# Performance work log

Hardware: AMD Instinct MI355X
Metric: run time of the kernel (lower is better)

## Reference

```python
import jax, jax.numpy as jnp
import numpy as np
import math

N = 50_000       # points (CSR segments)
V = 500_000      # mapped views (ragged rows)
IN_MAIN, IN_MAP, IN_MOD = 64, 16, 128
NC, NC_QK = 32, 8
EPS = 1e-12


def setup_inputs() -> dict:
    key = jax.random.key(0)
    ks = jax.random.split(key, 18)
    def rn(k, shape, fan_in=None):
        s = (1.0 / math.sqrt(fan_in)) if fan_in else 1.0
        return jax.random.normal(k, shape, jnp.float32) * s
    x_main = rn(ks[0], (N, IN_MAIN))
    x_mod = rn(ks[1], (V, IN_MOD))
    x_map = rn(ks[2], (V, IN_MAP))
    # CSR pointers: monotone, csr[0]=0, csr[-1]=V (full row coverage)
    inner = jnp.sort(jax.random.randint(ks[3], (N - 1,), 0, V))
    csr_idx = jnp.concatenate([jnp.zeros(1, jnp.int32), inner.astype(jnp.int32),
                               jnp.full((1,), V, jnp.int32)])
    return {
        "x_main": x_main, "x_mod": x_mod, "x_map": x_map, "csr_idx": csr_idx,
        # E_main: MLP([in_main, nc, nc], bias=False)
        "W_main1": rn(ks[4], (IN_MAIN, NC), IN_MAIN),
        "W_main2": rn(ks[5], (NC, NC), NC),
        # E_map (DeepSetFeat): elementwise MLP + segment-max set context + fuse
        "W_map1": rn(ks[6], (IN_MAP, NC), IN_MAP),
        "W_map2": rn(ks[7], (2 * NC, NC), 2 * NC),
        # E_mod: MLP([in_mod, in_mod, in_mod], bias=False)
        "W_mod1": rn(ks[8], (IN_MOD, IN_MOD), IN_MOD),
        "W_mod2": rn(ks[9], (IN_MOD, IN_MOD), IN_MOD),
        # Q, K linear heads (nc_inner -> nc_qk * num_groups), with bias
        "WQ": rn(ks[10], (NC, NC_QK), NC), "bQ": jnp.zeros((NC_QK,), jnp.float32),
        "WK": rn(ks[11], (NC, NC_QK), NC), "bK": jnp.zeros((NC_QK,), jnp.float32),
        # Gating(num_groups=1): weight init ones, bias init zeros
        "g_w": jnp.ones((1, 1), jnp.float32), "g_b": jnp.zeros((1, 1), jnp.float32),
    }


def reference(x_main, x_mod, x_map, csr_idx,
              W_main1, W_main2, W_map1, W_map2, W_mod1, W_mod2,
              WQ, bQ, WK, bK, g_w, g_b):
    counts = csr_idx[1:] - csr_idx[:-1]                     # [N]
    dense_idx = jnp.repeat(jnp.arange(N, dtype=jnp.int32), counts,
                           total_repeat_length=V)           # [V]
    nonempty = counts > 0                                   # [N]

    # --- encoders ---
    h_main = jax.nn.relu(x_main @ W_main1) @ W_main2        # [N, NC]
    h = jax.nn.relu(x_map @ W_map1)                         # [V, NC]
    set_ctx = jax.ops.segment_max(h, dense_idx, num_segments=N)
    set_ctx = jnp.where(nonempty[:, None], set_ctx, 0.0)    # empty segs -> 0
    h_map = jax.nn.relu(jnp.concatenate([h, set_ctx[dense_idx]], axis=1) @ W_map2)  # [V, NC]
    h_mod = jax.nn.relu(x_mod @ W_mod1) @ W_mod2            # [V, IN_MOD]

    # --- Q/K compatibilities (num_groups=1) ---
    keys = h_map @ WK + bK                                  # [V, NC_QK]
    queries = (h_main @ WQ + bQ)[dense_idx]                 # [V, NC_QK]
    comp = jnp.sum(keys * queries, axis=1) / jnp.sqrt(jnp.float32(NC_QK))  # [V]

    # --- segment_softmax_csr ---
    seg_max = jax.ops.segment_max(comp, dense_idx, num_segments=N)
    seg_max = jnp.where(nonempty, seg_max, 0.0)
    cexp = jnp.exp(comp - seg_max[dense_idx])               # [V]
    seg_sum = jax.ops.segment_sum(cexp, dense_idx, num_segments=N) + EPS
    att = cexp / seg_sum[dense_idx]                         # [V]

    # --- attention-weighted pooling ---
    x_pool = jax.ops.segment_sum(h_mod * att[:, None], dense_idx, num_segments=N)  # [N, IN_MOD]

    # --- gating on per-segment max compatibility ---
    gate_in = jnp.where(nonempty, seg_max, 0.0)[:, None]    # [N, 1]
    gate = jnp.tanh(jax.nn.relu(g_w * gate_in + g_b))       # [N, 1]
    x_pool = x_pool * gate

    x_seen = nonempty
    return x_pool, x_seen
```

## Files before the change

### kernel.cpp

```cpp
#include <hip/hip_runtime.h>
#include <math.h>

#define N_PTS 50000
#define V_VIEWS 500000
#define IN_MAIN 64
#define IN_MAP 16
#define IN_MOD 128
#define NC 32
#define NC_QK 8
#define SEG_EPS 1e-12f

typedef short bf16x8 __attribute__((ext_vector_type(8)));
typedef float f32x4 __attribute__((ext_vector_type(4)));

static __device__ __forceinline__ short f2bf(float x) {
    union { float f; unsigned u; } v; v.f = x;
    unsigned r = v.u + 0x7fffu + ((v.u >> 16) & 1u);
    return (short)(r >> 16);
}


__global__ __launch_bounds__(256) void k0_setup(const int* __restrict__ csr,
                                                const float* __restrict__ Wmod1,
                                                const float* __restrict__ Wmod2,
                                                const float* __restrict__ Wm1,
                                                const float* __restrict__ Wm2,
                                                int* __restrict__ didx,
                                                float* __restrict__ pooled,
                                                float* __restrict__ ctxw,
                                                short* __restrict__ Wf,
                                                short* __restrict__ W1f,
                                                short* __restrict__ W2af,
                                                short* __restrict__ W2f) {
    int t = blockIdx.x * blockDim.x + threadIdx.x;
    int total = gridDim.x * blockDim.x;
    if (t < N_PTS) {
        int a = csr[t], b = csr[t + 1];
        for (int v = a; v < b; ++v) didx[v] = t;
    }
    for (int i = t; i < N_PTS * IN_MOD; i += total) pooled[i] = 0.f;
    for (int i = t; i < N_PTS * NC; i += total) ctxw[i] = 0.f;
    for (int i = t; i < IN_MOD * IN_MOD; i += total) {
        int e = i & 7, l = (i >> 3) & 63, j = (i >> 9) & 7, kk = i >> 12;
        int k = kk * 32 + ((l >> 4) << 3) + e;
        int ch = (j << 4) + (l & 15);
        Wf[i] = f2bf(Wmod1[k * IN_MOD + ch]);
        W2f[i] = f2bf(Wmod2[k * IN_MOD + ch]);
    }
    for (int i = t; i < 1024; i += total) {
        int e = i & 7, l = (i >> 3) & 63, j = i >> 9;
        int k = ((l >> 4) << 3) + e;
        int ch = (j << 4) + (l & 15);
        W1f[i] = (k < IN_MAP) ? f2bf(Wm1[k * NC + ch]) : (short)0;
        W2af[i] = f2bf(Wm2[k * NC + ch]);
    }
}

__global__ __launch_bounds__(256) void kA_main_q(
    const float* __restrict__ x_main, const float* __restrict__ W1,
    const float* __restrict__ W2, const float* __restrict__ WQ,
    const float* __restrict__ bQ, const float* __restrict__ WK,
    const float* __restrict__ bK,
    float* __restrict__ wq, float* __restrict__ qb) {
    __shared__ float W1l[IN_MAIN * NC];
    __shared__ float W2l[NC * NC];
    __shared__ float WQl[NC * NC_QK];
    __shared__ float WKl[NC * NC_QK];
    __shared__ float bQl[NC_QK];
    __shared__ float bKl[NC_QK];
    __shared__ float h1buf[8][NC];
    __shared__ float h2buf[8][NC];
    __shared__ float qbuf[8][NC_QK];
    int tid = threadIdx.x;
    for (int i = tid; i < IN_MAIN * NC; i += 256) W1l[i] = W1[i];
    for (int i = tid; i < NC * NC; i += 256) W2l[i] = W2[i];
    for (int i = tid; i < NC * NC_QK; i += 256) WQl[i] = WQ[i];
    for (int i = tid; i < NC * NC_QK; i += 256) WKl[i] = WK[i];
    if (tid < NC_QK) { bQl[tid] = bQ[tid]; bKl[tid] = bK[tid]; }
    __syncthreads();
    int g = tid >> 5, c = tid & 31;
    int p = blockIdx.x * 8 + g;
    float h1 = 0.f;
    if (p < N_PTS) {
        const float* xr = x_main + (size_t)p * IN_MAIN;
        for (int k = 0; k < IN_MAIN; ++k) h1 += xr[k] * W1l[k * NC + c];
        h1 = fmaxf(h1, 0.f);
    }
    h1buf[g][c] = h1;
    __syncthreads();
    float h2 = 0.f;
    for (int j = 0; j < NC; ++j) h2 += h1buf[g][j] * W2l[j * NC + c];
    h2buf[g][c] = h2;
    __syncthreads();
    if (c < NC_QK) {
        float acc = bQl[c];
        for (int j = 0; j < NC; ++j) acc += h2buf[g][j] * WQl[j * NC_QK + c];
        qbuf[g][c] = acc;
    }
    __syncthreads();
    if (p < N_PTS) {
        float w = 0.f;
        for (int j = 0; j < NC_QK; ++j) w += WKl[c * NC_QK + j] * qbuf[g][j];
        wq[(size_t)p * NC + c] = w;
        if (c == 0) {
            float b = 0.f;
            for (int j = 0; j < NC_QK; ++j) b += bKl[j] * qbuf[g][j];
            qb[p] = b;
        }
    }
}

__global__ __launch_bounds__(256) void kH_ctx(
    const float* __restrict__ x_map, const int* __restrict__ didx,
    const short* __restrict__ W1f, int* __restrict__ ctxbits,
    short* __restrict__ hbuf) {
    __shared__ float hl[4][16 * 36];
    int tid = threadIdx.x;
    int w = tid >> 6, lane = tid & 63;
    int vbase = blockIdx.x * 64 + w * 16;
    if (vbase >= V_VIEWS) return;
    const bf16x8* pW1 = (const bf16x8*)W1f;
    bf16x8 b1a = pW1[lane], b1b = pW1[64 + lane];

    bf16x8 a1 = (bf16x8){0, 0, 0, 0, 0, 0, 0, 0};
    if (lane < 32) {
        const float* xp = x_map + (size_t)(vbase + (lane & 15)) * IN_MAP + ((lane >> 4) << 3);
        float4 x0 = *(const float4*)xp;
        float4 x1 = *(const float4*)(xp + 4);
        a1[0] = f2bf(x0.x); a1[1] = f2bf(x0.y); a1[2] = f2bf(x0.z); a1[3] = f2bf(x0.w);
        a1[4] = f2bf(x1.x); a1[5] = f2bf(x1.y); a1[6] = f2bf(x1.z); a1[7] = f2bf(x1.w);
    }
    f32x4 d1a = (f32x4){0.f, 0.f, 0.f, 0.f}, d1b = (f32x4){0.f, 0.f, 0.f, 0.f};
    d1a = __builtin_amdgcn_mfma_f32_16x16x32_bf16(a1, b1a, d1a, 0, 0, 0);
    d1b = __builtin_amdgcn_mfma_f32_16x16x32_bf16(a1, b1b, d1b, 0, 0, 0);

    int c = lane & 15, kq = lane >> 4;
    int vr0 = kq << 2;
    float* hw = hl[w];
#pragma unroll
    for (int r = 0; r < 4; ++r) {
        hw[(vr0 + r) * 36 + c] = fmaxf(d1a[r], 0.f);
        hw[(vr0 + r) * 36 + c + 16] = fmaxf(d1b[r], 0.f);
    }
    const float* hr = hw + c * 36 + (kq << 3);
    float4 h0 = *(const float4*)hr;
    float4 h1 = *(const float4*)(hr + 4);
    bf16x8 a2;
    a2[0] = f2bf(h0.x); a2[1] = f2bf(h0.y); a2[2] = f2bf(h0.z); a2[3] = f2bf(h0.w);
    a2[4] = f2bf(h1.x); a2[5] = f2bf(h1.y); a2[6] = f2bf(h1.z); a2[7] = f2bf(h1.w);
    *(bf16x8*)(hbuf + (size_t)(vbase + c) * NC + (kq << 3)) = a2;

    int vg = vbase + vr0;
    int4 ss = *(const int4*)(didx + vg);
    const int* sp = (const int*)&ss;
    float ma = 0.f, mb = 0.f;
#pragma unroll
    for (int r = 0; r < 4; ++r) {
        ma = fmaxf(ma, fmaxf(d1a[r], 0.f));
        mb = fmaxf(mb, fmaxf(d1b[r], 0.f));
        bool runend = (r == 3) || (sp[r + 1] != sp[r]);
        if (runend) {
            atomicMax(&ctxbits[sp[r] * NC + c], __float_as_int(ma));
            atomicMax(&ctxbits[sp[r] * NC + c + 16], __float_as_int(mb));
            ma = 0.f; mb = 0.f;
        }
    }
}

__global__ __launch_bounds__(256) void kB2b_ctxw(
    const float* __restrict__ Wm2, float* __restrict__ ctxw) {
    __shared__ float W2bl[NC * NC];
    __shared__ float ctxl[8][NC];
    int tid = threadIdx.x;
    for (int i = tid; i < NC * NC; i += 256) W2bl[i] = Wm2[NC * NC + i];
    int g = tid >> 5, c = tid & 31;
    int s = blockIdx.x * 8 + g;
    float cv = (s < N_PTS) ? ctxw[(size_t)s * NC + c] : 0.f;
    ctxl[g][c] = cv;
    __syncthreads();
    if (s < N_PTS) {
        float val = 0.f;
        for (int j = 0; j < NC; ++j) val += ctxl[g][j] * W2bl[j * NC + c];
        ctxw[(size_t)s * NC + c] = val;
    }
}

__global__ __launch_bounds__(256) void kB3_comp(
    const short* __restrict__ hbuf, const int* __restrict__ didx,
    const short* __restrict__ W2af,
    const float* __restrict__ ctxW2b, const float* __restrict__ wq,
    const float* __restrict__ qb, float* __restrict__ comp) {
    int tid = threadIdx.x;
    int w = tid >> 6, lane = tid & 63;
    int vbase = blockIdx.x * 64 + w * 16;
    if (vbase >= V_VIEWS) return;
    const bf16x8* pW2 = (const bf16x8*)W2af;
    bf16x8 b2a = pW2[lane], b2b = pW2[64 + lane];
    int c = lane & 15, kq = lane >> 4;

    bf16x8 a2 = *(const bf16x8*)(hbuf + (size_t)(vbase + c) * NC + (kq << 3));
    f32x4 d2a = (f32x4){0.f, 0.f, 0.f, 0.f}, d2b = (f32x4){0.f, 0.f, 0.f, 0.f};
    d2a = __builtin_amdgcn_mfma_f32_16x16x32_bf16(a2, b2a, d2a, 0, 0, 0);
    d2b = __builtin_amdgcn_mfma_f32_16x16x32_bf16(a2, b2b, d2b, 0, 0, 0);

    int vr0 = kq << 2;
    int vg = vbase + vr0;
    int4 ss = *(const int4*)(didx + vg);
    const int* sp = (const int*)&ss;
    float part[4];
#pragma unroll
    for (int r = 0; r < 4; ++r) {
        size_t so = (size_t)sp[r] * NC;
        float m0 = fmaxf(d2a[r] + ctxW2b[so + c], 0.f);
        float m1 = fmaxf(d2b[r] + ctxW2b[so + c + 16], 0.f);
        part[r] = m0 * wq[so + c] + m1 * wq[so + c + 16];
    }
#pragma unroll
    for (int mask = 1; mask < 16; mask <<= 1) {
#pragma unroll
        for (int r = 0; r < 4; ++r) part[r] += __shfl_xor(part[r], mask);
    }
    if (c == 0) {
        const float inv_sqrt = 0.35355339059327373f;
        float4 o;
        o.x = (part[0] + qb[sp[0]]) * inv_sqrt;
        o.y = (part[1] + qb[sp[1]]) * inv_sqrt;
        o.z = (part[2] + qb[sp[2]]) * inv_sqrt;
        o.w = (part[3] + qb[sp[3]]) * inv_sqrt;
        *(float4*)(comp + vg) = o;
    }
}

__global__ __launch_bounds__(256) void kB4_att(
    const float* __restrict__ comp, const int* __restrict__ csr,
    float* __restrict__ segmax, float* __restrict__ invsum) {
    int wid = threadIdx.x >> 6, lane = threadIdx.x & 63;
    int seg = blockIdx.x * 4 + wid;
    if (seg >= N_PTS) return;
    int v0 = csr[seg], v1 = csr[seg + 1];
    if (v0 >= v1) {
        if (lane == 0) { segmax[seg] = 0.f; invsum[seg] = 0.f; }
        return;
    }
    float mx = -__builtin_inff();
    for (int v = v0 + lane; v < v1; v += 64) mx = fmaxf(mx, comp[v]);
    for (int o = 32; o > 0; o >>= 1) mx = fmaxf(mx, __shfl_xor(mx, o));
    float sm = 0.f;
    for (int v = v0 + lane; v < v1; v += 64) sm += __expf(comp[v] - mx);
    for (int o = 32; o > 0; o >>= 1) sm += __shfl_xor(sm, o);
    if (lane == 0) { segmax[seg] = mx; invsum[seg] = 1.f / (sm + SEG_EPS); }
}

#define VB 64
__global__ __launch_bounds__(256) void kC_pool(
    const float* __restrict__ x_mod, const short* __restrict__ Wf,
    const int* __restrict__ didx, const int* __restrict__ csr,
    const float* __restrict__ comp, const float* __restrict__ segmax,
    const float* __restrict__ invsum, float* __restrict__ pooled) {
    __shared__ float Yl[VB * 132];
    __shared__ float attl[VB];
    __shared__ int didxl[VB];
    int tid = threadIdx.x;
    int vbase = blockIdx.x * VB;
    if (tid < VB) {
        int v = vbase + tid;
        if (v < V_VIEWS) {
            int s = didx[v];
            didxl[tid] = s;
            attl[tid] = __expf(comp[v] - segmax[s]) * invsum[s];
        } else {
            didxl[tid] = didx[V_VIEWS - 1];
            attl[tid] = 0.f;
        }
    }
    __syncthreads();

    int w = tid >> 6, lane = tid & 63;
    int row16 = lane & 15;
    int kq = lane >> 4;
    int k0 = kq << 3;
    f32x4 acc[8];
    for (int j = 0; j < 8; ++j) acc[j] = (f32x4){0.f, 0.f, 0.f, 0.f};

    int v = vbase + w * 16 + row16;
    if (v >= V_VIEWS) v = V_VIEWS - 1;
    const float* xp = x_mod + (size_t)v * IN_MOD;

#pragma unroll
    for (int kk = 0; kk < 4; ++kk) {
        float4 x0 = *(const float4*)(xp + kk * 32 + k0);
        float4 x1 = *(const float4*)(xp + kk * 32 + k0 + 4);
        bf16x8 a;
        a[0] = f2bf(x0.x); a[1] = f2bf(x0.y); a[2] = f2bf(x0.z); a[3] = f2bf(x0.w);
        a[4] = f2bf(x1.x); a[5] = f2bf(x1.y); a[6] = f2bf(x1.z); a[7] = f2bf(x1.w);
        const bf16x8* wf = (const bf16x8*)(Wf + ((size_t)(kk * 8) * 64 + lane) * 8);
#pragma unroll
        for (int j = 0; j < 8; ++j) {
            bf16x8 b = wf[j * 64];
            acc[j] = __builtin_amdgcn_mfma_f32_16x16x32_bf16(a, b, acc[j], 0, 0, 0);
        }
    }
#pragma unroll
    for (int j = 0; j < 8; ++j) {
        int ch = j * 16 + row16;
        int rbase = w * 16 + (kq << 2);
#pragma unroll
        for (int r = 0; r < 4; ++r) {
            int rw = rbase + r;
            Yl[rw * 132 + ch] = fmaxf(acc[j][r], 0.f) * attl[rw];
        }
    }
    __syncthreads();
    {
        int halfid = tid >> 7, cc = tid & 127;
        int r0 = halfid << 5;
        int hb = vbase + r0;
        float s_acc = 0.f;
        int cur = didxl[r0];
        for (int r = r0; r < r0 + 32; ++r) {
            int s = didxl[r];
            if (s != cur) {
                if (csr[cur] >= hb && csr[cur + 1] <= hb + 32)
                    pooled[(size_t)cur * IN_MOD + cc] = s_acc;
                else
                    atomicAdd(&pooled[(size_t)cur * IN_MOD + cc], s_acc);
                s_acc = 0.f; cur = s;
            }
            s_acc += Yl[r * 132 + cc];
        }
        if (csr[cur] >= hb && csr[cur + 1] <= hb + 32)
            pooled[(size_t)cur * IN_MOD + cc] = s_acc;
        else
            atomicAdd(&pooled[(size_t)cur * IN_MOD + cc], s_acc);
    }
}

__global__ __launch_bounds__(256) void kD_final(
    const short* __restrict__ W2f,
    const float* __restrict__ segmax, const int* __restrict__ csr,
    const float* __restrict__ g_w, const float* __restrict__ g_b,
    float* __restrict__ out) {
    int tid = threadIdx.x;
    int w = tid >> 6, lane = tid & 63;
    int row16 = lane & 15;
    int kq = lane >> 4;
    int k0 = kq << 3;
    int rbase = blockIdx.x * 64 + w * 16;
    float gw = g_w[0], gb = g_b[0];

    int rr = rbase + row16;
    if (rr >= N_PTS) rr = N_PTS - 1;
    const float* xp = out + (size_t)rr * IN_MOD;

    f32x4 acc[8];
    for (int j = 0; j < 8; ++j) acc[j] = (f32x4){0.f, 0.f, 0.f, 0.f};
#pragma unroll
    for (int kk = 0; kk < 4; ++kk) {
        float4 x0 = *(const float4*)(xp + kk * 32 + k0);
        float4 x1 = *(const float4*)(xp + kk * 32 + k0 + 4);
        bf16x8 a;
        a[0] = f2bf(x0.x); a[1] = f2bf(x0.y); a[2] = f2bf(x0.z); a[3] = f2bf(x0.w);
        a[4] = f2bf(x1.x); a[5] = f2bf(x1.y); a[6] = f2bf(x1.z); a[7] = f2bf(x1.w);
        const bf16x8* wf = (const bf16x8*)(W2f + ((size_t)(kk * 8) * 64 + lane) * 8);
#pragma unroll
        for (int j = 0; j < 8; ++j) {
            bf16x8 b = wf[j * 64];
            acc[j] = __builtin_amdgcn_mfma_f32_16x16x32_bf16(a, b, acc[j], 0, 0, 0);
        }
    }
    float gate[4];
    int rowv[4];
#pragma unroll
    for (int r = 0; r < 4; ++r) {
        int ro = rbase + (kq << 2) + r;
        rowv[r] = ro;
        if (ro < N_PTS) {
            bool nz = csr[ro + 1] > csr[ro];
            float gin = nz ? segmax[ro] : 0.f;
            gate[r] = tanhf(fmaxf(gw * gin + gb, 0.f));
            if (row16 == 0) out[(size_t)N_PTS * IN_MOD + ro] = nz ? 1.f : 0.f;
        } else {
            gate[r] = 0.f;
        }
    }
#pragma unroll
    for (int j = 0; j < 8; ++j) {
        int ch = j * 16 + row16;
#pragma unroll
        for (int r = 0; r < 4; ++r) {
            if (rowv[r] < N_PTS)
                out[(size_t)rowv[r] * IN_MOD + ch] = acc[j][r] * gate[r];
        }
    }
}

extern "C" void kernel_launch(void* const* d_in, const int* in_sizes, int n_in,
                              void* d_out, int out_size, void* d_ws, size_t ws_size,
                              hipStream_t stream) {
    (void)in_sizes; (void)n_in; (void)out_size; (void)ws_size;
    const float* x_main = (const float*)d_in[0];
    const float* x_mod  = (const float*)d_in[1];
    const float* x_map  = (const float*)d_in[2];
    const int*   csr    = (const int*)d_in[3];
    const float* W_main1 = (const float*)d_in[4];
    const float* W_main2 = (const float*)d_in[5];
    const float* W_map1  = (const float*)d_in[6];
    const float* W_map2  = (const float*)d_in[7];
    const float* W_mod1  = (const float*)d_in[8];
    const float* W_mod2  = (const float*)d_in[9];
    const float* WQ = (const float*)d_in[10];
    const float* bQ = (const float*)d_in[11];
    const float* WK = (const float*)d_in[12];
    const float* bK = (const float*)d_in[13];
    const float* g_w = (const float*)d_in[14];
    const float* g_b = (const float*)d_in[15];
    float* out = (float*)d_out;

    char* ws = (char*)d_ws;
    int*   didx   = (int*)ws;
    float* wq     = (float*)(ws + 2000000);
    float* qb     = (float*)(ws + 8400000);
    float* ctxw   = (float*)(ws + 8600000);
    float* comp   = (float*)(ws + 15000000);
    float* segmax = (float*)(ws + 17000000);
    short* Wf     = (short*)(ws + 17200000);
    short* W1f    = (short*)(ws + 17240000);
    short* W2af   = (short*)(ws + 17244000);
    short* W2f    = (short*)(ws + 17248000);
    float* invsum = (float*)(ws + 17300000);
    short* hbuf   = (short*)(ws + 17500000);
    float* pooled = out;

    k0_setup<<<512, 256, 0, stream>>>(csr, W_mod1, W_mod2, W_map1, W_map2,
                                      didx, pooled, ctxw, Wf, W1f, W2af, W2f);
    kA_main_q<<<(N_PTS + 7) / 8, 256, 0, stream>>>(x_main, W_main1, W_main2, WQ, bQ,
                                                   WK, bK, wq, qb);
    kH_ctx<<<(V_VIEWS + 63) / 64, 256, 0, stream>>>(x_map, didx, W1f, (int*)ctxw, hbuf);
    kB2b_ctxw<<<(N_PTS + 7) / 8, 256, 0, stream>>>(W_map2, ctxw);
    kB3_comp<<<(V_VIEWS + 63) / 64, 256, 0, stream>>>(hbuf, didx, W2af,
                                                      ctxw, wq, qb, comp);
    kB4_att<<<(N_PTS + 3) / 4, 256, 0, stream>>>(comp, csr, segmax, invsum);
    kC_pool<<<(V_VIEWS + VB - 1) / VB, 256, 0, stream>>>(x_mod, Wf, didx, csr,
                                                         comp, segmax, invsum, pooled);
    kD_final<<<(N_PTS + 63) / 64, 256, 0, stream>>>(W2f, segmax, csr, g_w, g_b, out);
}
```

Baseline: 235.4 us.

## Fuse per-view encoders, softmax and pooling into segment-aligned blocks

Replaces the chain of per-view kernels (context max, ctx projection, compatibility, segment softmax, pooling) with one kernel. Each block owns the whole CSR segments that start in a 64-view window, found by a binary search folded into the main-encoder kernel. Intermediates (h, context, compat, attention) stay in shared memory, and pooled rows are written directly, so global atomics, the dense index buffer and the zero-init pass all go away. The trade-offs are fixed shared-memory capacities (HCAP/SEGCAP) that assume bounded segment sizes, serial per-thread softmax and reduction loops, and bf16 rounding of the weighted rows before summation.

```diff
diff --git a/kernel.cpp b/kernel.cpp
--- a/kernel.cpp
+++ b/kernel.cpp
@@ -10,6 +10,12 @@
 #define NC_QK 8
 #define SEG_EPS 1e-12f
 
+#define WWIN 64
+#define NBLK ((V_VIEWS + WWIN - 1) / WWIN)
+#define HCAP 320
+#define SEGCAP 48
+#define KA_BLOCKS ((N_PTS + 7) / 8)
+
 typedef short bf16x8 __attribute__((ext_vector_type(8)));
 typedef float f32x4 __attribute__((ext_vector_type(4)));
 
@@ -18,50 +24,21 @@
     unsigned r = v.u + 0x7fffu + ((v.u >> 16) & 1u);
     return (short)(r >> 16);
 }
-
-
-__global__ __launch_bounds__(256) void k0_setup(const int* __restrict__ csr,
-                                                const float* __restrict__ Wmod1,
-                                                const float* __restrict__ Wmod2,
-                                                const float* __restrict__ Wm1,
-                                                const float* __restrict__ Wm2,
-                                                int* __restrict__ didx,
-                                                float* __restrict__ pooled,
-                                                float* __restrict__ ctxw,
-                                                short* __restrict__ Wf,
-                                                short* __restrict__ W1f,
-                                                short* __restrict__ W2af,
-                                                short* __restrict__ W2f) {
-    int t = blockIdx.x * blockDim.x + threadIdx.x;
-    int total = gridDim.x * blockDim.x;
-    if (t < N_PTS) {
-        int a = csr[t], b = csr[t + 1];
-        for (int v = a; v < b; ++v) didx[v] = t;
-    }
-    for (int i = t; i < N_PTS * IN_MOD; i += total) pooled[i] = 0.f;
-    for (int i = t; i < N_PTS * NC; i += total) ctxw[i] = 0.f;
-    for (int i = t; i < IN_MOD * IN_MOD; i += total) {
-        int e = i & 7, l = (i >> 3) & 63, j = (i >> 9) & 7, kk = i >> 12;
-        int k = kk * 32 + ((l >> 4) << 3) + e;
-        int ch = (j << 4) + (l & 15);
-        Wf[i] = f2bf(Wmod1[k * IN_MOD + ch]);
-        W2f[i] = f2bf(Wmod2[k * IN_MOD + ch]);
-    }
-    for (int i = t; i < 1024; i += total) {
-        int e = i & 7, l = (i >> 3) & 63, j = i >> 9;
-        int k = ((l >> 4) << 3) + e;
-        int ch = (j << 4) + (l & 15);
-        W1f[i] = (k < IN_MAP) ? f2bf(Wm1[k * NC + ch]) : (short)0;
-        W2af[i] = f2bf(Wm2[k * NC + ch]);
-    }
-}
-
-__global__ __launch_bounds__(256) void kA_main_q(
+static __device__ __forceinline__ float bf2f(unsigned short b) {
+    union { unsigned u; float f; } v; v.u = ((unsigned)b) << 16; return v.f;
+}
+
+
+__global__ __launch_bounds__(256) void kA0(
     const float* __restrict__ x_main, const float* __restrict__ W1,
     const float* __restrict__ W2, const float* __restrict__ WQ,
     const float* __restrict__ bQ, const float* __restrict__ WK,
-    const float* __restrict__ bK,
-    float* __restrict__ wq, float* __restrict__ qb) {
+    const float* __restrict__ bK, const int* __restrict__ csr,
+    const float* __restrict__ Wmod1, const float* __restrict__ Wmod2,
+    const float* __restrict__ Wm1, const float* __restrict__ Wm2,
+    float* __restrict__ wq, float* __restrict__ qb, int* __restrict__ S,
+    short* __restrict__ Wf, short* __restrict__ W1f,
+    short* __restrict__ W2af, short* __restrict__ W2f) {
     __shared__ float W1l[IN_MAIN * NC];
     __shared__ float W2l[NC * NC];
     __shared__ float WQl[NC * NC_QK];
@@ -108,230 +85,221 @@
             qb[p] = b;
         }
     }
-}
-
-__global__ __launch_bounds__(256) void kH_ctx(
-    const float* __restrict__ x_map, const int* __restrict__ didx,
-    const short* __restrict__ W1f, int* __restrict__ ctxbits,
-    short* __restrict__ hbuf) {
-    __shared__ float hl[4][16 * 36];
+    int gt = blockIdx.x * 256 + tid;
+    int gtotal = gridDim.x * 256;
+    for (int b = gt; b <= NBLK; b += gtotal) {
+        int target = b * WWIN;
+        int lo = 0, hi = N_PTS;
+        while (lo < hi) { int mid = (lo + hi) >> 1; if (csr[mid] < target) lo = mid + 1; else hi = mid; }
+        S[b] = lo;
+    }
+    for (int i = gt; i < IN_MOD * IN_MOD; i += gtotal) {
+        int e = i & 7, l = (i >> 3) & 63, j = (i >> 9) & 7, kk = i >> 12;
+        int k = kk * 32 + ((l >> 4) << 3) + e;
+        int ch = (j << 4) + (l & 15);
+        Wf[i] = f2bf(Wmod1[k * IN_MOD + ch]);
+        W2f[i] = f2bf(Wmod2[k * IN_MOD + ch]);
+    }
+    for (int i = gt; i < 1024; i += gtotal) {
+        int e = i & 7, l = (i >> 3) & 63, j = i >> 9;
+        int k = ((l >> 4) << 3) + e;
+        int ch = (j << 4) + (l & 15);
+        W1f[i] = (k < IN_MAP) ? f2bf(Wm1[k * NC + ch]) : (short)0;
+        W2af[i] = f2bf(Wm2[k * NC + ch]);
+    }
+}
+
+__global__ __launch_bounds__(256) void kSEG(
+    const float* __restrict__ x_map, const float* __restrict__ x_mod,
+    const int* __restrict__ csr, const int* __restrict__ S,
+    const short* __restrict__ W1f, const short* __restrict__ W2af,
+    const short* __restrict__ Wf, const float* __restrict__ Wm2,
+    const float* __restrict__ wq, const float* __restrict__ qb,
+    float* __restrict__ segmax_g, float* __restrict__ pooled) {
+    __shared__ short hls[HCAP * 40];
+    __shared__ float ctxl[SEGCAP * 33];
+    __shared__ float ctxw2[SEGCAP * 33];
+    __shared__ float wql[SEGCAP * 33];
+    __shared__ float qbl[SEGCAP];
+    __shared__ float attl[HCAP + 16];
+    __shared__ short didxl[HCAP];
+    __shared__ int csrl[SEGCAP + 1];
+    __shared__ float W2bl[NC * 33];
+
     int tid = threadIdx.x;
+    int S0 = S[blockIdx.x], S1 = S[blockIdx.x + 1];
+    if (S0 >= S1) return;
+    int nseg = S1 - S0;
+    for (int i = tid; i <= nseg; i += 256) csrl[i] = csr[S0 + i];
+    for (int i = tid; i < NC * NC; i += 256) W2bl[(i >> 5) * 33 + (i & 31)] = Wm2[NC * NC + i];
+    for (int i = tid; i < nseg * NC; i += 256) {
+        wql[(i >> 5) * 33 + (i & 31)] = wq[(size_t)(S0 + (i >> 5)) * NC + (i & 31)];
+        ctxl[(i >> 5) * 33 + (i & 31)] = 0.f;
+    }
+    for (int i = tid; i < nseg; i += 256) qbl[i] = qb[S0 + i];
+    __syncthreads();
+    int v0 = csrl[0], v1 = csrl[nseg];
+    int nv = v1 - v0;
+    for (int j = tid; j < nseg; j += 256)
+        for (int v = csrl[j]; v < csrl[j + 1]; ++v) didxl[v - v0] = (short)j;
+    __syncthreads();
+
     int w = tid >> 6, lane = tid & 63;
-    int vbase = blockIdx.x * 64 + w * 16;
-    if (vbase >= V_VIEWS) return;
+    int c = lane & 15, kq = lane >> 4;
     const bf16x8* pW1 = (const bf16x8*)W1f;
+    const bf16x8* pW2 = (const bf16x8*)W2af;
     bf16x8 b1a = pW1[lane], b1b = pW1[64 + lane];
-
-    bf16x8 a1 = (bf16x8){0, 0, 0, 0, 0, 0, 0, 0};
-    if (lane < 32) {
-        const float* xp = x_map + (size_t)(vbase + (lane & 15)) * IN_MAP + ((lane >> 4) << 3);
-        float4 x0 = *(const float4*)xp;
-        float4 x1 = *(const float4*)(xp + 4);
-        a1[0] = f2bf(x0.x); a1[1] = f2bf(x0.y); a1[2] = f2bf(x0.z); a1[3] = f2bf(x0.w);
-        a1[4] = f2bf(x1.x); a1[5] = f2bf(x1.y); a1[6] = f2bf(x1.z); a1[7] = f2bf(x1.w);
-    }
-    f32x4 d1a = (f32x4){0.f, 0.f, 0.f, 0.f}, d1b = (f32x4){0.f, 0.f, 0.f, 0.f};
-    d1a = __builtin_amdgcn_mfma_f32_16x16x32_bf16(a1, b1a, d1a, 0, 0, 0);
-    d1b = __builtin_amdgcn_mfma_f32_16x16x32_bf16(a1, b1b, d1b, 0, 0, 0);
-
-    int c = lane & 15, kq = lane >> 4;
-    int vr0 = kq << 2;
-    float* hw = hl[w];
-#pragma unroll
-    for (int r = 0; r < 4; ++r) {
-        hw[(vr0 + r) * 36 + c] = fmaxf(d1a[r], 0.f);
-        hw[(vr0 + r) * 36 + c + 16] = fmaxf(d1b[r], 0.f);
-    }
-    const float* hr = hw + c * 36 + (kq << 3);
-    float4 h0 = *(const float4*)hr;
-    float4 h1 = *(const float4*)(hr + 4);
-    bf16x8 a2;
-    a2[0] = f2bf(h0.x); a2[1] = f2bf(h0.y); a2[2] = f2bf(h0.z); a2[3] = f2bf(h0.w);
-    a2[4] = f2bf(h1.x); a2[5] = f2bf(h1.y); a2[6] = f2bf(h1.z); a2[7] = f2bf(h1.w);
-    *(bf16x8*)(hbuf + (size_t)(vbase + c) * NC + (kq << 3)) = a2;
-
-    int vg = vbase + vr0;
-    int4 ss = *(const int4*)(didx + vg);
-    const int* sp = (const int*)&ss;
-    float ma = 0.f, mb = 0.f;
-#pragma unroll
-    for (int r = 0; r < 4; ++r) {
-        ma = fmaxf(ma, fmaxf(d1a[r], 0.f));
-        mb = fmaxf(mb, fmaxf(d1b[r], 0.f));
-        bool runend = (r == 3) || (sp[r + 1] != sp[r]);
-        if (runend) {
-            atomicMax(&ctxbits[sp[r] * NC + c], __float_as_int(ma));
-            atomicMax(&ctxbits[sp[r] * NC + c + 16], __float_as_int(mb));
-            ma = 0.f; mb = 0.f;
-        }
-    }
-}
-
-__global__ __launch_bounds__(256) void kB2b_ctxw(
-    const float* __restrict__ Wm2, float* __restrict__ ctxw) {
-    __shared__ float W2bl[NC * NC];
-    __shared__ float ctxl[8][NC];
-    int tid = threadIdx.x;
-    for (int i = tid; i < NC * NC; i += 256) W2bl[i] = Wm2[NC * NC + i];
-    int g = tid >> 5, c = tid & 31;
-    int s = blockIdx.x * 8 + g;
-    float cv = (s < N_PTS) ? ctxw[(size_t)s * NC + c] : 0.f;
-    ctxl[g][c] = cv;
-    __syncthreads();
-    if (s < N_PTS) {
+    bf16x8 b2a = pW2[lane], b2b = pW2[64 + lane];
+
+    for (int t = w; t * 16 < nv; t += 4) {
+        int row0 = t * 16;
+        bf16x8 a1 = (bf16x8){0, 0, 0, 0, 0, 0, 0, 0};
+        if (lane < 32) {
+            int vv = v0 + row0 + (lane & 15);
+            if (vv >= V_VIEWS) vv = V_VIEWS - 1;
+            const float* xp = x_map + (size_t)vv * IN_MAP + ((lane >> 4) << 3);
+            float4 x0 = *(const float4*)xp;
+            float4 x1 = *(const float4*)(xp + 4);
+            a1[0] = f2bf(x0.x); a1[1] = f2bf(x0.y); a1[2] = f2bf(x0.z); a1[3] = f2bf(x0.w);
+            a1[4] = f2bf(x1.x); a1[5] = f2bf(x1.y); a1[6] = f2bf(x1.z); a1[7] = f2bf(x1.w);
+        }
+        f32x4 d1a = (f32x4){0.f, 0.f, 0.f, 0.f}, d1b = (f32x4){0.f, 0.f, 0.f, 0.f};
+        d1a = __builtin_amdgcn_mfma_f32_16x16x32_bf16(a1, b1a, d1a, 0, 0, 0);
+        d1b = __builtin_amdgcn_mfma_f32_16x16x32_bf16(a1, b1b, d1b, 0, 0, 0);
+        int vr0 = kq << 2;
+#pragma unroll
+        for (int r = 0; r < 4; ++r) {
+            int rw = row0 + vr0 + r;
+            hls[rw * 40 + c] = f2bf(fmaxf(d1a[r], 0.f));
+            hls[rw * 40 + c + 16] = f2bf(fmaxf(d1b[r], 0.f));
+        }
+        float ma = 0.f, mb = 0.f;
+        int pj = -1;
+#pragma unroll
+        for (int r = 0; r < 4; ++r) {
+            int rw = row0 + vr0 + r;
+            if (rw < nv) {
+                int j = didxl[rw];
+                if (j != pj) {
+                    if (pj >= 0) {
+                        atomicMax((int*)&ctxl[pj * 33 + c], __float_as_int(ma));
+                        atomicMax((int*)&ctxl[pj * 33 + c + 16], __float_as_int(mb));
+                    }
+                    ma = 0.f; mb = 0.f; pj = j;
+                }
+                ma = fmaxf(ma, fmaxf(d1a[r], 0.f));
+                mb = fmaxf(mb, fmaxf(d1b[r], 0.f));
+            }
+        }
+        if (pj >= 0) {
+            atomicMax((int*)&ctxl[pj * 33 + c], __float_as_int(ma));
+            atomicMax((int*)&ctxl[pj * 33 + c + 16], __float_as_int(mb));
+        }
+    }
+    __syncthreads();
+    for (int idx = tid; idx < nseg * NC; idx += 256) {
+        int j = idx >> 5, cp = idx & 31;
         float val = 0.f;
-        for (int j = 0; j < NC; ++j) val += ctxl[g][j] * W2bl[j * NC + c];
-        ctxw[(size_t)s * NC + c] = val;
-    }
-}
-
-__global__ __launch_bounds__(256) void kB3_comp(
-    const short* __restrict__ hbuf, const int* __restrict__ didx,
-    const short* __restrict__ W2af,
-    const float* __restrict__ ctxW2b, const float* __restrict__ wq,
-    const float* __restrict__ qb, float* __restrict__ comp) {
-    int tid = threadIdx.x;
-    int w = tid >> 6, lane = tid & 63;
-    int vbase = blockIdx.x * 64 + w * 16;
-    if (vbase >= V_VIEWS) return;
-    const bf16x8* pW2 = (const bf16x8*)W2af;
-    bf16x8 b2a = pW2[lane], b2b = pW2[64 + lane];
-    int c = lane & 15, kq = lane >> 4;
-
-    bf16x8 a2 = *(const bf16x8*)(hbuf + (size_t)(vbase + c) * NC + (kq << 3));
-    f32x4 d2a = (f32x4){0.f, 0.f, 0.f, 0.f}, d2b = (f32x4){0.f, 0.f, 0.f, 0.f};
-    d2a = __builtin_amdgcn_mfma_f32_16x16x32_bf16(a2, b2a, d2a, 0, 0, 0);
-    d2b = __builtin_amdgcn_mfma_f32_16x16x32_bf16(a2, b2b, d2b, 0, 0, 0);
-
-    int vr0 = kq << 2;
-    int vg = vbase + vr0;
-    int4 ss = *(const int4*)(didx + vg);
-    const int* sp = (const int*)&ss;
-    float part[4];
-#pragma unroll
-    for (int r = 0; r < 4; ++r) {
-        size_t so = (size_t)sp[r] * NC;
-        float m0 = fmaxf(d2a[r] + ctxW2b[so + c], 0.f);
-        float m1 = fmaxf(d2b[r] + ctxW2b[so + c + 16], 0.f);
-        part[r] = m0 * wq[so + c] + m1 * wq[so + c + 16];
-    }
-#pragma unroll
-    for (int mask = 1; mask < 16; mask <<= 1) {
-#pragma unroll
-        for (int r = 0; r < 4; ++r) part[r] += __shfl_xor(part[r], mask);
-    }
-    if (c == 0) {
-        const float inv_sqrt = 0.35355339059327373f;
-        float4 o;
-        o.x = (part[0] + qb[sp[0]]) * inv_sqrt;
-        o.y = (part[1] + qb[sp[1]]) * inv_sqrt;
-        o.z = (part[2] + qb[sp[2]]) * inv_sqrt;
-        o.w = (part[3] + qb[sp[3]]) * inv_sqrt;
-        *(float4*)(comp + vg) = o;
-    }
-}
-
-__global__ __launch_bounds__(256) void kB4_att(
-    const float* __restrict__ comp, const int* __restrict__ csr,
-    float* __restrict__ segmax, float* __restrict__ invsum) {
-    int wid = threadIdx.x >> 6, lane = threadIdx.x & 63;
-    int seg = blockIdx.x * 4 + wid;
-    if (seg >= N_PTS) return;
-    int v0 = csr[seg], v1 = csr[seg + 1];
-    if (v0 >= v1) {
-        if (lane == 0) { segmax[seg] = 0.f; invsum[seg] = 0.f; }
-        return;
-    }
-    float mx = -__builtin_inff();
-    for (int v = v0 + lane; v < v1; v += 64) mx = fmaxf(mx, comp[v]);
-    for (int o = 32; o > 0; o >>= 1) mx = fmaxf(mx, __shfl_xor(mx, o));
-    float sm = 0.f;
-    for (int v = v0 + lane; v < v1; v += 64) sm += __expf(comp[v] - mx);
-    for (int o = 32; o > 0; o >>= 1) sm += __shfl_xor(sm, o);
-    if (lane == 0) { segmax[seg] = mx; invsum[seg] = 1.f / (sm + SEG_EPS); }
-}
-
-#define VB 64
-__global__ __launch_bounds__(256) void kC_pool(
-    const float* __restrict__ x_mod, const short* __restrict__ Wf,
-    const int* __restrict__ didx, const int* __restrict__ csr,
-    const float* __restrict__ comp, const float* __restrict__ segmax,
-    const float* __restrict__ invsum, float* __restrict__ pooled) {
-    __shared__ float Yl[VB * 132];
-    __shared__ float attl[VB];
-    __shared__ int didxl[VB];
-    int tid = threadIdx.x;
-    int vbase = blockIdx.x * VB;
-    if (tid < VB) {
-        int v = vbase + tid;
-        if (v < V_VIEWS) {
-            int s = didx[v];
-            didxl[tid] = s;
-            attl[tid] = __expf(comp[v] - segmax[s]) * invsum[s];
-        } else {
-            didxl[tid] = didx[V_VIEWS - 1];
-            attl[tid] = 0.f;
-        }
-    }
-    __syncthreads();
-
-    int w = tid >> 6, lane = tid & 63;
-    int row16 = lane & 15;
-    int kq = lane >> 4;
-    int k0 = kq << 3;
-    f32x4 acc[8];
-    for (int j = 0; j < 8; ++j) acc[j] = (f32x4){0.f, 0.f, 0.f, 0.f};
-
-    int v = vbase + w * 16 + row16;
-    if (v >= V_VIEWS) v = V_VIEWS - 1;
-    const float* xp = x_mod + (size_t)v * IN_MOD;
-
-#pragma unroll
-    for (int kk = 0; kk < 4; ++kk) {
-        float4 x0 = *(const float4*)(xp + kk * 32 + k0);
-        float4 x1 = *(const float4*)(xp + kk * 32 + k0 + 4);
-        bf16x8 a;
-        a[0] = f2bf(x0.x); a[1] = f2bf(x0.y); a[2] = f2bf(x0.z); a[3] = f2bf(x0.w);
-        a[4] = f2bf(x1.x); a[5] = f2bf(x1.y); a[6] = f2bf(x1.z); a[7] = f2bf(x1.w);
-        const bf16x8* wf = (const bf16x8*)(Wf + ((size_t)(kk * 8) * 64 + lane) * 8);
-#pragma unroll
-        for (int j = 0; j < 8; ++j) {
-            bf16x8 b = wf[j * 64];
-            acc[j] = __builtin_amdgcn_mfma_f32_16x16x32_bf16(a, b, acc[j], 0, 0, 0);
-        }
-    }
-#pragma unroll
-    for (int j = 0; j < 8; ++j) {
-        int ch = j * 16 + row16;
-        int rbase = w * 16 + (kq << 2);
+        for (int k = 0; k < NC; ++k) val += ctxl[j * 33 + k] * W2bl[k * 33 + cp];
+        ctxw2[j * 33 + cp] = val;
+    }
+    __syncthreads();
+    for (int t = w; t * 16 < nv; t += 4) {
+        int row0 = t * 16;
+        bf16x8 a2 = *(const bf16x8*)&hls[(row0 + c) * 40 + (kq << 3)];
+        f32x4 d2a = (f32x4){0.f, 0.f, 0.f, 0.f}, d2b = (f32x4){0.f, 0.f, 0.f, 0.f};
+        d2a = __builtin_amdgcn_mfma_f32_16x16x32_bf16(a2, b2a, d2a, 0, 0, 0);
+        d2b = __builtin_amdgcn_mfma_f32_16x16x32_bf16(a2, b2b, d2b, 0, 0, 0);
+        int vr0 = kq << 2;
+        float part[4];
+        int jj[4];
 #pragma unroll
         for (int r = 0; r < 4; ++r) {
-            int rw = rbase + r;
-            Yl[rw * 132 + ch] = fmaxf(acc[j][r], 0.f) * attl[rw];
-        }
-    }
-    __syncthreads();
-    {
-        int halfid = tid >> 7, cc = tid & 127;
-        int r0 = halfid << 5;
-        int hb = vbase + r0;
+            int rw = row0 + vr0 + r;
+            int j = (rw < nv) ? (int)didxl[rw] : 0;
+            jj[r] = j;
+            float m0 = fmaxf(d2a[r] + ctxw2[j * 33 + c], 0.f);
+            float m1 = fmaxf(d2b[r] + ctxw2[j * 33 + c + 16], 0.f);
+            part[r] = m0 * wql[j * 33 + c] + m1 * wql[j * 33 + c + 16];
+        }
+#pragma unroll
+        for (int mask = 1; mask < 16; mask <<= 1) {
+#pragma unroll
+            for (int r = 0; r < 4; ++r) part[r] += __shfl_xor(part[r], mask);
+        }
+        if (c == 0) {
+#pragma unroll
+            for (int r = 0; r < 4; ++r) {
+                int rw = row0 + vr0 + r;
+                if (rw < nv) attl[rw] = (part[r] + qbl[jj[r]]) * 0.35355339059327373f;
+            }
+        }
+    }
+    __syncthreads();
+    for (int j = tid; j < nseg; j += 256) {
+        int a = csrl[j] - v0, e = csrl[j + 1] - v0;
+        if (a >= e) { segmax_g[S0 + j] = 0.f; continue; }
+        float m = attl[a];
+        for (int r = a + 1; r < e; ++r) m = fmaxf(m, attl[r]);
+        float smv = 0.f;
+        for (int r = a; r < e; ++r) smv += __expf(attl[r] - m);
+        float inv = 1.f / (smv + SEG_EPS);
+        for (int r = a; r < e; ++r) attl[r] = __expf(attl[r] - m) * inv;
+        segmax_g[S0 + j] = m;
+    }
+    __syncthreads();
+    if (nv > 0) {
+        unsigned short* Ybl = (unsigned short*)hls;
         float s_acc = 0.f;
-        int cur = didxl[r0];
-        for (int r = r0; r < r0 + 32; ++r) {
-            int s = didxl[r];
-            if (s != cur) {
-                if (csr[cur] >= hb && csr[cur + 1] <= hb + 32)
-                    pooled[(size_t)cur * IN_MOD + cc] = s_acc;
-                else
-                    atomicAdd(&pooled[(size_t)cur * IN_MOD + cc], s_acc);
-                s_acc = 0.f; cur = s;
+        int cur_j = didxl[0];
+        for (int c0 = 0; c0 < nv; c0 += 64) {
+            int row0 = c0 + w * 16;
+            int vv = v0 + row0 + (lane & 15);
+            if (vv >= V_VIEWS) vv = V_VIEWS - 1;
+            const float* xp = x_mod + (size_t)vv * IN_MOD;
+            f32x4 acc[8];
+            for (int j = 0; j < 8; ++j) acc[j] = (f32x4){0.f, 0.f, 0.f, 0.f};
+#pragma unroll
+            for (int kk = 0; kk < 4; ++kk) {
+                float4 x0 = *(const float4*)(xp + kk * 32 + (kq << 3));
+                float4 x1 = *(const float4*)(xp + kk * 32 + (kq << 3) + 4);
+                bf16x8 a;
+                a[0] = f2bf(x0.x); a[1] = f2bf(x0.y); a[2] = f2bf(x0.z); a[3] = f2bf(x0.w);
+                a[4] = f2bf(x1.x); a[5] = f2bf(x1.y); a[6] = f2bf(x1.z); a[7] = f2bf(x1.w);
+                const bf16x8* wf = (const bf16x8*)(Wf + ((size_t)(kk * 8) * 64 + lane) * 8);
+#pragma unroll
+                for (int j = 0; j < 8; ++j) {
+                    bf16x8 b = wf[j * 64];
+                    acc[j] = __builtin_amdgcn_mfma_f32_16x16x32_bf16(a, b, acc[j], 0, 0, 0);
+                }
             }
-            s_acc += Yl[r * 132 + cc];
-        }
-        if (csr[cur] >= hb && csr[cur + 1] <= hb + 32)
-            pooled[(size_t)cur * IN_MOD + cc] = s_acc;
-        else
-            atomicAdd(&pooled[(size_t)cur * IN_MOD + cc], s_acc);
+#pragma unroll
+            for (int j = 0; j < 8; ++j) {
+                int ch = j * 16 + (lane & 15);
+                int rb = w * 16 + (kq << 2);
+#pragma unroll
+                for (int r = 0; r < 4; ++r) {
+                    int rwl = rb + r;
+                    int rwg = c0 + rwl;
+                    float av = (rwg < nv) ? attl[rwg] : 0.f;
+                    Ybl[rwl * 160 + ch] = (unsigned short)f2bf(fmaxf(acc[j][r], 0.f) * av);
+                }
+            }
+            __syncthreads();
+            if (tid < 128) {
+                int rend = (c0 + 64 < nv) ? c0 + 64 : nv;
+                for (int r = c0; r < rend; ++r) {
+                    int j = didxl[r];
+                    if (j != cur_j) {
+                        pooled[(size_t)(S0 + cur_j) * IN_MOD + tid] = s_acc;
+                        s_acc = 0.f; cur_j = j;
+                    }
+                    s_acc += bf2f(Ybl[(r - c0) * 160 + tid]);
+                }
+            }
+            __syncthreads();
+        }
+        if (tid < 128) pooled[(size_t)(S0 + cur_j) * IN_MOD + tid] = s_acc;
     }
 }
 
@@ -417,30 +385,20 @@
     float* out = (float*)d_out;
 
     char* ws = (char*)d_ws;
-    int*   didx   = (int*)ws;
-    float* wq     = (float*)(ws + 2000000);
-    float* qb     = (float*)(ws + 8400000);
-    float* ctxw   = (float*)(ws + 8600000);
-    float* comp   = (float*)(ws + 15000000);
-    float* segmax = (float*)(ws + 17000000);
-    short* Wf     = (short*)(ws + 17200000);
-    short* W1f    = (short*)(ws + 17240000);
-    short* W2af   = (short*)(ws + 17244000);
-    short* W2f    = (short*)(ws + 17248000);
-    float* invsum = (float*)(ws + 17300000);
-    short* hbuf   = (short*)(ws + 17500000);
+    float* wq     = (float*)ws;
+    float* qb     = (float*)(ws + 6400000);
+    float* segmax = (float*)(ws + 6700000);
+    int*   S      = (int*)(ws + 7000000);
+    short* Wf     = (short*)(ws + 7100000);
+    short* W1f    = (short*)(ws + 7140000);
+    short* W2af   = (short*)(ws + 7144000);
+    short* W2f    = (short*)(ws + 7148000);
     float* pooled = out;
 
-    k0_setup<<<512, 256, 0, stream>>>(csr, W_mod1, W_mod2, W_map1, W_map2,
-                                      didx, pooled, ctxw, Wf, W1f, W2af, W2f);
-    kA_main_q<<<(N_PTS + 7) / 8, 256, 0, stream>>>(x_main, W_main1, W_main2, WQ, bQ,
-                                                   WK, bK, wq, qb);
-    kH_ctx<<<(V_VIEWS + 63) / 64, 256, 0, stream>>>(x_map, didx, W1f, (int*)ctxw, hbuf);
-    kB2b_ctxw<<<(N_PTS + 7) / 8, 256, 0, stream>>>(W_map2, ctxw);
-    kB3_comp<<<(V_VIEWS + 63) / 64, 256, 0, stream>>>(hbuf, didx, W2af,
-                                                      ctxw, wq, qb, comp);
-    kB4_att<<<(N_PTS + 3) / 4, 256, 0, stream>>>(comp, csr, segmax, invsum);
-    kC_pool<<<(V_VIEWS + VB - 1) / VB, 256, 0, stream>>>(x_mod, Wf, didx, csr,
-                                                         comp, segmax, invsum, pooled);
+    kA0<<<KA_BLOCKS, 256, 0, stream>>>(x_main, W_main1, W_main2, WQ, bQ, WK, bK, csr,
+                                       W_mod1, W_mod2, W_map1, W_map2,
+                                       wq, qb, S, Wf, W1f, W2af, W2f);
+    kSEG<<<NBLK, 256, 0, stream>>>(x_map, x_mod, csr, S, W1f, W2af, Wf, W_map2,
+                                   wq, qb, segmax, pooled);
     kD_final<<<(N_PTS + 63) / 64, 256, 0, stream>>>(W2f, segmax, csr, g_w, g_b, out);
 }
```

Measured after the change: 422.2 us. 79.4% more time.
